# Kernel tuning notes

Measured on AMD Instinct MI355X. Metric: run time of the kernel, lower is better.

The kernel has to match this reference:

```python
import jax, jax.numpy as jnp
import numpy as np
import math

D = 300      # input_size
H = 5        # gat heads
NLAYERS = 2  # txt_gat_layer == img_gat_layer
N, L, K = 64, 1024, 64
E_TXT, E_IMG = 2048, 512


def _gat(x, edge_index, W, att_src, att_dst, bias):
    """PyG GATConv, concat=False (head mean), no self loops, eval mode (no dropout).
    x: (n, D); edge_index: (2, E); W: (D, H, D); att_*: (H, D); bias: (D,)."""
    n = x.shape[0]
    h = jnp.einsum('ld,dhe->lhe', x, W)                    # (n, H, D)
    src, dst = edge_index[0], edge_index[1]
    a_src = jnp.sum(h * att_src, axis=-1)                  # (n, H)
    a_dst = jnp.sum(h * att_dst, axis=-1)                  # (n, H)
    e = jax.nn.leaky_relu(a_src[src] + a_dst[dst], 0.2)    # (E, H)
    m = jax.ops.segment_max(e, dst, num_segments=n)        # per-target max
    m = jnp.where(jnp.isfinite(m), m, 0.0)                 # nodes w/o in-edges
    p = jnp.exp(e - m[dst])
    denom = jax.ops.segment_sum(p, dst, num_segments=n)
    alpha = p / (denom[dst] + 1e-16)                       # (E, H)
    out = jax.ops.segment_sum(alpha[:, :, None] * h[src], dst, num_segments=n)
    return out.mean(axis=1) + bias                         # (n, D)


def _layer_norm(x, g, b):
    mu = jnp.mean(x, axis=-1, keepdims=True)
    var = jnp.mean((x - mu) ** 2, axis=-1, keepdims=True)
    return (x - mu) / jnp.sqrt(var + 1e-5) * g + b


def _forward(t2, v2, score, edge_index, gnn_mask, key_padding_mask, np_mask,
             img_edge_index, txt_W, txt_att_src, txt_att_dst, txt_bias,
             img_W, img_att_src, img_att_dst, img_bias,
             w1, b1, w2, b2, ln_g, ln_b, lam=1.0):
    scale = 1.0 / jnp.sqrt(jnp.asarray(D, t2.dtype))
    q1 = jnp.einsum('nld,nkd->nlk', t2, v2) * scale        # (N, L, K)
    c = jnp.sum(score * t2, axis=1, keepdims=True)         # (N, 1, D)
    pa_token = t2 @ w1 + b1                                # (N, L)
    pa_token = jnp.where(key_padding_mask, -jnp.inf, pa_token)

    gat_txt = jax.vmap(_gat, in_axes=(0, 0, None, None, None, None))
    tnp = t2
    for i in range(NLAYERS):
        g = gat_txt(tnp, edge_index, txt_W[i], txt_att_src[i], txt_att_dst[i], txt_bias[i])
        g = jnp.where(gnn_mask[:, None, None], 0.0, g)     # masked graph -> zeros
        tnp = _layer_norm(jax.nn.relu(g), ln_g, ln_b)

    gat_img = jax.vmap(_gat, in_axes=(0, None, None, None, None, None))
    v3 = v2
    for i in range(NLAYERS):
        g = gat_img(v3, img_edge_index, img_W[i], img_att_src[i], img_att_dst[i], img_bias[i])
        v3 = _layer_norm(jax.nn.relu(g), ln_g, ln_b)

    tnp = jnp.concatenate([tnp, c], axis=1)                # (N, L+1, D)
    q2 = jnp.einsum('nld,nkd->nlk', tnp, v3) * scale       # (N, L+1, K)
    pa_np = tnp @ w2 + b2                                  # (N, L+1)
    pa_np = jnp.where(np_mask, -jnp.inf, pa_np)
    pa_np = jax.nn.softmax(pa_np * lam, axis=1)
    pa_tok = jax.nn.softmax(pa_token * lam, axis=1)
    a1 = jnp.sum(q1 * pa_tok[:, :, None], axis=1)          # (N, K)
    a2 = jnp.sum(q2 * pa_np[:, :, None], axis=1)           # (N, K)
    return jnp.concatenate([a1, a2], axis=1)               # (N, 2K)


def setup_inputs() -> dict:
    key = jax.random.key(0)
    ks = jax.random.split(key, 24)
    ws = 1.0 / math.sqrt(D)
    return {
        't2': jax.random.normal(ks[0], (N, L, D), jnp.float32),
        'v2': jax.random.normal(ks[1], (N, K, D), jnp.float32),
        'score': jax.random.uniform(ks[2], (N, L, D), jnp.float32),
        'edge_index': jax.random.randint(ks[3], (N, 2, E_TXT), 0, L),
        'gnn_mask': jnp.zeros((N,), bool),
        'key_padding_mask': jax.random.bernoulli(ks[4], 0.1, (N, L)),
        'np_mask': jax.random.bernoulli(ks[5], 0.1, (N, L + 1)),
        'img_edge_index': jax.random.randint(ks[6], (2, E_IMG), 0, K),
        'txt_W': jax.random.normal(ks[7], (NLAYERS, D, H, D), jnp.float32) * ws,
        'txt_att_src': jax.random.normal(ks[8], (NLAYERS, H, D), jnp.float32) * 0.1,
        'txt_att_dst': jax.random.normal(ks[9], (NLAYERS, H, D), jnp.float32) * 0.1,
        'txt_bias': jnp.zeros((NLAYERS, D), jnp.float32),
        'img_W': jax.random.normal(ks[10], (NLAYERS, D, H, D), jnp.float32) * ws,
        'img_att_src': jax.random.normal(ks[11], (NLAYERS, H, D), jnp.float32) * 0.1,
        'img_att_dst': jax.random.normal(ks[12], (NLAYERS, H, D), jnp.float32) * 0.1,
        'img_bias': jnp.zeros((NLAYERS, D), jnp.float32),
        'w1': jax.random.normal(ks[13], (D,), jnp.float32) * ws,
        'b1': jnp.zeros((), jnp.float32),
        'w2': jax.random.normal(ks[14], (D,), jnp.float32) * ws,
        'b2': jnp.zeros((), jnp.float32),
        'ln_g': jnp.ones((D,), jnp.float32),
        'ln_b': jnp.zeros((D,), jnp.float32),
    }


def reference(t2, v2, score, edge_index, gnn_mask, key_padding_mask, np_mask,
              img_edge_index, txt_W, txt_att_src, txt_att_dst, txt_bias,
              img_W, img_att_src, img_att_dst, img_bias,
              w1, b1, w2, b2, ln_g, ln_b):
    return _forward(t2, v2, score, edge_index, gnn_mask, key_padding_mask, np_mask,
                    img_edge_index, txt_W, txt_att_src, txt_att_dst, txt_bias,
                    img_W, img_att_src, img_att_dst, img_bias,
                    w1, b1, w2, b2, ln_g, ln_b)
```

## Files before the change

### kernel.cpp

```cpp
#include <hip/hip_runtime.h>
#include <hip/hip_bf16.h>
#include <math.h>

typedef __hip_bfloat16 bf16;
__device__ __forceinline__ float toF(float v){ return v; }
__device__ __forceinline__ float toF(bf16 v){ return __bfloat162float(v); }
__device__ __forceinline__ bf16 f2bf(float v){ return __float2bfloat16(v); }

#define D_    300
#define H_    5
#define NB    64
#define LL    1024
#define KK    64
#define ETXT  2048
#define EIMG  512
#define MAXDEG 128
#define KP    320
#define NP    1536

typedef __attribute__((ext_vector_type(8))) short short8;
typedef __attribute__((ext_vector_type(4))) float f32x4;

__device__ __forceinline__ int read_mask(const void* p, int i, int mode) {
  switch (mode) {
    case 1: return ((const unsigned short*)p)[i] != 0;
    case 2: return ((const unsigned char*)p)[i] != 0;
    case 3: { const unsigned int* w = (const unsigned int*)p;
              return (w[2*i] | w[2*i+1]) != 0; }
    default: return ((const unsigned int*)p)[i] != 0;
  }
}

__global__ void k_detect(const unsigned int* __restrict__ w, int nwords,
                         int* __restrict__ mode) {
  __shared__ unsigned int se[256], so[256];
  unsigned int oe = 0, oo = 0;
  for (int i = threadIdx.x; i < nwords; i += 256) {
    unsigned int v = w[i];
    if (i & 1) oo |= v; else oe |= v;
  }
  se[threadIdx.x] = oe; so[threadIdx.x] = oo;
  __syncthreads();
  for (int s = 128; s; s >>= 1) {
    if (threadIdx.x < s) { se[threadIdx.x] |= se[threadIdx.x+s]; so[threadIdx.x] |= so[threadIdx.x+s]; }
    __syncthreads();
  }
  if (threadIdx.x == 0) {
    unsigned int O = se[0] | so[0];
    int m = 0;
    if (O == 0u) m = 0;
    else if ((O & 0xFFFFu) == 0x3F80u) m = 1;
    else if ((O >> 16) == 0x3F80u && (O & 0xFFFFu) == 0u) m = 0;
    else if ((O >> 16) == 0x3FF0u) m = 3;
    else if (O <= 1u) m = (so[0] == 0u && se[0] != 0u) ? 3 : 0;
    else if ((O & 0xFEFEFEFEu) == 0u) m = 2;
    mode[0] = m;
  }
}

__global__ __launch_bounds__(256) void k_csr(const int* __restrict__ edges, int estride,
                                             int E, int nodes,
                                             int* __restrict__ rowptr, int rstride,
                                             int* __restrict__ col, int cstride) {
  int g = blockIdx.x, tid = threadIdx.x;
  __shared__ int cnt[1025];
  __shared__ int psum[257];
  const int* src = edges + (size_t)g * estride;
  const int* dst = src + E;
  for (int i = tid; i <= nodes; i += 256) cnt[i] = 0;
  __syncthreads();
  for (int e = tid; e < E; e += 256) atomicAdd(&cnt[dst[e]], 1);
  __syncthreads();
  int base = tid * 4;
  int loc = 0;
#pragma unroll
  for (int i = 0; i < 4; ++i) { int idx = base + i; if (idx < nodes) loc += cnt[idx]; }
  psum[tid + 1] = loc;
  if (tid == 0) psum[0] = 0;
  __syncthreads();
  if (tid == 0) { for (int i = 1; i <= 256; ++i) psum[i] += psum[i - 1]; }
  __syncthreads();
  int run = psum[tid];
  int starts[4];
#pragma unroll
  for (int i = 0; i < 4; ++i) {
    int idx = base + i;
    if (idx < nodes) { int c = cnt[idx]; starts[i] = run; run += c; }
  }
  __syncthreads();
#pragma unroll
  for (int i = 0; i < 4; ++i) {
    int idx = base + i;
    if (idx < nodes) { cnt[idx] = starts[i]; rowptr[(size_t)g * rstride + idx] = starts[i]; }
  }
  if (tid == 0) rowptr[(size_t)g * rstride + nodes] = E;
  __syncthreads();
  for (int e = tid; e < E; e += 256) {
    int pos = atomicAdd(&cnt[dst[e]], 1);
    col[(size_t)g * cstride + pos] = src[e];
  }
}

__global__ __launch_bounds__(1024) void k_c_part(const float* __restrict__ t2,
                                                 const float* __restrict__ score,
                                                 float* __restrict__ cpart) {
  int n = blockIdx.x, part = blockIdx.y;
  int lane = threadIdx.x & 63, ty = threadIdx.x >> 6;
  __shared__ float red[16][304];
  float acc[5] = {0.f, 0.f, 0.f, 0.f, 0.f};
  int l0 = part * 256;
  for (int l = l0 + ty; l < l0 + 256; l += 16) {
    const float* tp = t2 + ((size_t)n * LL + l) * D_;
    const float* sp = score + ((size_t)n * LL + l) * D_;
#pragma unroll
    for (int j = 0; j < 5; ++j) { int d = lane + 64 * j; if (d < D_) acc[j] += tp[d] * sp[d]; }
  }
#pragma unroll
  for (int j = 0; j < 5; ++j) { int d = lane + 64 * j; if (d < D_) red[ty][d] = acc[j]; }
  __syncthreads();
  for (int d = threadIdx.x; d < D_; d += 1024) {
    float s = 0.f;
#pragma unroll
    for (int t = 0; t < 16; ++t) s += red[t][d];
    cpart[((size_t)part * NB + n) * D_ + d] = s;
  }
}

__global__ void k_c_red(const float* __restrict__ cpart, float* __restrict__ c) {
  int idx = blockIdx.x * 256 + threadIdx.x;
  if (idx >= NB * D_) return;
  const int S = NB * D_;
  c[idx] = cpart[idx] + cpart[S + idx] + cpart[2 * S + idx] + cpart[3 * S + idx];
}

__device__ __forceinline__ float clamp_logit(float v) {
  if (!(v > -1e30f)) v = -1e30f;
  if (v > 1e30f) v = 1e30f;
  return v;
}

__global__ void k_logits_tok(const float* __restrict__ x, const float* __restrict__ w,
                             const float* __restrict__ b, const void* __restrict__ mask,
                             const int* __restrict__ mmode,
                             float* __restrict__ logits, int rows) {
  int row = blockIdx.x * blockDim.y + threadIdx.y;
  if (row >= rows) return;
  int lane = threadIdx.x;
  const float* xp = x + (size_t)row * D_;
  float acc = 0.f;
  for (int d = lane; d < D_; d += 64) acc += xp[d] * w[d];
#pragma unroll
  for (int off = 32; off; off >>= 1) acc += __shfl_down(acc, off);
  if (lane == 0) {
    float v = clamp_logit(acc + b[0]);
    if (read_mask(mask, row, mmode[0])) v = -INFINITY;
    logits[row] = v;
  }
}

__global__ void k_logits_np(const bf16* __restrict__ X, const float* __restrict__ c,
                            const float* __restrict__ w, const float* __restrict__ b,
                            const void* __restrict__ mask, const int* __restrict__ mmode,
                            float* __restrict__ logits) {
  int row = blockIdx.x * blockDim.y + threadIdx.y;
  if (row >= NB * (LL + 1)) return;
  int n = row / (LL + 1), l = row % (LL + 1);
  int lane = threadIdx.x;
  float acc = 0.f;
  if (l < LL) {
    const char* xp = (const char*)(X + ((size_t)n * LL + l) * D_);
#pragma unroll
    for (int t = 0; t < 3; ++t) {
      int d2 = lane + 64 * t;
      if (d2 < 150) {
        unsigned int u = *(const unsigned int*)(xp + d2 * 4);
        float2 wv = *(const float2*)&w[d2 * 2];
        acc += __uint_as_float(u << 16) * wv.x + __uint_as_float(u & 0xFFFF0000u) * wv.y;
      }
    }
  } else {
    const float* cp = c + n * D_;
    for (int d = lane; d < D_; d += 64) acc += cp[d] * w[d];
  }
#pragma unroll
  for (int off = 32; off; off >>= 1) acc += __shfl_down(acc, off);
  if (lane == 0) {
    float v = clamp_logit(acc + b[0]);
    if (read_mask(mask, row, mmode[0])) v = -INFINITY;
    logits[row] = v;
  }
}

__global__ __launch_bounds__(1024) void k_pa(const float* __restrict__ lg1,
                                             const float* __restrict__ lg2,
                                             float* __restrict__ pa1,
                                             float* __restrict__ pa2) {
  int b = blockIdx.x, tid = threadIdx.x;
  int which = b >> 6, n = b & 63;
  const float* lg = which ? (lg2 + (size_t)n * (LL + 1)) : (lg1 + (size_t)n * LL);
  float* pa = which ? (pa2 + (size_t)n * (LL + 1)) : (pa1 + (size_t)n * LL);
  __shared__ float red[16];
  __shared__ float stat;
  float v0 = lg[tid];
  float vx = (which && tid == 0) ? lg[LL] : -INFINITY;
  float m = fmaxf(v0, vx);
#pragma unroll
  for (int off = 32; off; off >>= 1) m = fmaxf(m, __shfl_xor(m, off));
  if ((tid & 63) == 0) red[tid >> 6] = m;
  __syncthreads();
  if (tid == 0) {
    float mm = red[0];
    for (int i = 1; i < 16; ++i) mm = fmaxf(mm, red[i]);
    stat = mm;
  }
  __syncthreads();
  float M = stat;
  if (!(M > -INFINITY && M < INFINITY)) M = 0.f;
  float p0 = __expf(v0 - M);
  float px = (which && tid == 0) ? __expf(vx - M) : 0.f;
  float s = p0 + px;
#pragma unroll
  for (int off = 32; off; off >>= 1) s += __shfl_xor(s, off);
  __syncthreads();
  if ((tid & 63) == 0) red[tid >> 6] = s;
  __syncthreads();
  if (tid == 0) {
    float ss = 0.f;
    for (int i = 0; i < 16; ++i) ss += red[i];
    stat = ss;
  }
  __syncthreads();
  float inv = (stat > 0.f) ? 1.f / stat : 0.f;
  pa[tid] = p0 * inv;
  if (which && tid == 0) pa[LL] = px * inv;
}

__global__ __launch_bounds__(1024) void k_u1part(const float* __restrict__ pa1,
                                                 const float* __restrict__ t2,
                                                 float* __restrict__ up) {
  int n = blockIdx.x, part = blockIdx.y;
  int lane = threadIdx.x & 63, ty = threadIdx.x >> 6;
  __shared__ float red[16][304];
  float acc[5] = {0.f, 0.f, 0.f, 0.f, 0.f};
  const float* pw = pa1 + (size_t)n * LL;
  int l0 = part * 256;
  for (int l = l0 + ty; l < l0 + 256; l += 16) {
    float w = pw[l];
    const float* tp = t2 + ((size_t)n * LL + l) * D_;
#pragma unroll
    for (int j = 0; j < 5; ++j) { int d = lane + 64 * j; if (d < D_) acc[j] += w * tp[d]; }
  }
#pragma unroll
  for (int j = 0; j < 5; ++j) { int d = lane + 64 * j; if (d < D_) red[ty][d] = acc[j]; }
  __syncthreads();
  for (int d = threadIdx.x; d < D_; d += 1024) {
    float s = 0.f;
#pragma unroll
    for (int t = 0; t < 16; ++t) s += red[t][d];
    up[((size_t)part * NB + n) * D_ + d] = s;
  }
}

__global__ __launch_bounds__(1024) void k_u2part(const float* __restrict__ pa2,
                                                 const bf16* __restrict__ X,
                                                 const float* __restrict__ c,
                                                 float* __restrict__ up) {
  int n = blockIdx.x, part = blockIdx.y;
  int lane = threadIdx.x & 63, ty = threadIdx.x >> 6;
  __shared__ float red[16][304];
  float acc[3][2] = {};
  const float* pw = pa2 + (size_t)n * (LL + 1);
  int l0 = part * 256;
  for (int l = l0 + ty; l < l0 + 256; l += 16) {
    float w = pw[l];
    const char* xp = (const char*)(X + ((size_t)n * LL + l) * D_);
#pragma unroll
    for (int t = 0; t < 3; ++t) {
      int d2 = lane + 64 * t;
      if (d2 < 150) {
        unsigned int u = *(const unsigned int*)(xp + d2 * 4);
        acc[t][0] += w * __uint_as_float(u << 16);
        acc[t][1] += w * __uint_as_float(u & 0xFFFF0000u);
      }
    }
  }
#pragma unroll
  for (int t = 0; t < 3; ++t) {
    int d2 = lane + 64 * t;
    if (d2 < 150) { red[ty][d2 * 2] = acc[t][0]; red[ty][d2 * 2 + 1] = acc[t][1]; }
  }
  __syncthreads();
  for (int d = threadIdx.x; d < D_; d += 1024) {
    float s = 0.f;
#pragma unroll
    for (int t = 0; t < 16; ++t) s += red[t][d];
    if (part == 3) s += pw[LL] * c[(size_t)n * D_ + d];
    up[((size_t)part * NB + n) * D_ + d] = s;
  }
}

__global__ void k_ured(const float* __restrict__ up1, const float* __restrict__ up2,
                       float* __restrict__ u1, float* __restrict__ u2) {
  int idx = blockIdx.x * 256 + threadIdx.x;
  if (idx >= NB * D_) return;
  const int S = NB * D_;
  u1[idx] = up1[idx] + up1[S + idx] + up1[2 * S + idx] + up1[3 * S + idx];
  u2[idx] = up2[idx] + up2[S + idx] + up2[2 * S + idx] + up2[3 * S + idx];
}

__global__ void k_wvec(const float* __restrict__ W, const float* __restrict__ att_src,
                       const float* __restrict__ att_dst, float* __restrict__ wsrc,
                       float* __restrict__ wdst) {
  int idx = blockIdx.x * blockDim.x + threadIdx.x;
  if (idx >= 2 * H_ * D_) return;
  int s = idx / (H_ * D_);
  int r = idx % (H_ * D_);
  int h = r / D_, d = r % D_;
  const float* att = (s ? att_dst : att_src) + h * D_;
  const float* Wp = W + (size_t)d * H_ * D_ + h * D_;
  float acc = 0.f;
  for (int e = 0; e < D_; ++e) acc += Wp[e] * att[e];
  (s ? wdst : wsrc)[h * D_ + d] = acc;
}

template <typename T>
__global__ void k_asrc(const T* __restrict__ x, const float* __restrict__ wsrc,
                       const float* __restrict__ wdst, float* __restrict__ a_src,
                       float* __restrict__ a_dst, int rows) {
  int row = blockIdx.x * blockDim.y + threadIdx.y;
  if (row >= rows) return;
  int lane = threadIdx.x;
  float xr[3][2];
#pragma unroll
  for (int t = 0; t < 3; ++t) {
    int d2 = lane + 64 * t;
    if (d2 < 150) {
      if constexpr (sizeof(T) == 4) {
        float2 v = *(const float2*)((const float*)x + (size_t)row * D_ + d2 * 2);
        xr[t][0] = v.x; xr[t][1] = v.y;
      } else {
        unsigned int u = *(const unsigned int*)((const char*)x + ((size_t)row * D_) * 2 + d2 * 4);
        xr[t][0] = __uint_as_float(u << 16); xr[t][1] = __uint_as_float(u & 0xFFFF0000u);
      }
    } else { xr[t][0] = 0.f; xr[t][1] = 0.f; }
  }
#pragma unroll
  for (int hh = 0; hh < H_; ++hh) {
    float as = 0.f, ad = 0.f;
#pragma unroll
    for (int t = 0; t < 3; ++t) {
      int d2 = lane + 64 * t;
      if (d2 < 150) {
        float2 ws = *(const float2*)&wsrc[hh * D_ + d2 * 2];
        float2 wd = *(const float2*)&wdst[hh * D_ + d2 * 2];
        as += xr[t][0] * ws.x + xr[t][1] * ws.y;
        ad += xr[t][0] * wd.x + xr[t][1] * wd.y;
      }
    }
#pragma unroll
    for (int off = 32; off; off >>= 1) { as += __shfl_down(as, off); ad += __shfl_down(ad, off); }
    if (lane == 0) { a_src[(size_t)row * H_ + hh] = as; a_dst[(size_t)row * H_ + hh] = ad; }
  }
}

template <typename T>
__global__ void k_packA(const T* __restrict__ src, bf16* __restrict__ Ap, int M) {
  int idx = blockIdx.x * 256 + threadIdx.x;
  if (idx >= M * KP) return;
  int m = idx / KP, k = idx - m * KP;
  Ap[idx] = (k < D_) ? f2bf(toF(src[(size_t)m * D_ + k])) : f2bf(0.f);
}

__global__ void k_packB(const float* __restrict__ B, bf16* __restrict__ Bp) {
  int idx = blockIdx.x * 256 + threadIdx.x;
  if (idx >= NP * KP) return;
  int j = idx / KP, k = idx - j * KP;
  float v = (k < D_ && j < H_ * D_) ? B[(size_t)k * (H_ * D_) + j] : 0.f;
  Bp[idx] = f2bf(v);
}

__global__ __launch_bounds__(256) void k_gemm_mfma(const bf16* __restrict__ Ap,
                                                   const bf16* __restrict__ Bp,
                                                   bf16* __restrict__ C, int M, int nrow) {
  __shared__ short As[128][40];
  __shared__ short Bs[128][40];
  int b = blockIdx.x;
  int xcd = b & 7, j = b >> 3;
  int rg = xcd + 8 * (j / 12);
  if (rg >= nrow) return;
  int m0 = rg * 128, n0 = (j % 12) * 128;
  int tid = threadIdx.x;
  int wave = tid >> 6, lane = tid & 63;
  int wr = (wave >> 1) * 64, wc = (wave & 1) * 64;
  f32x4 acc[4][4] = {};
  for (int k0 = 0; k0 < KP; k0 += 32) {
#pragma unroll
    for (int cc = 0; cc < 2; ++cc) {
      int c = tid + cc * 256;
      int m = c >> 2, ko = (c & 3) << 3;
      int row = m0 + m; if (row >= M) row = M - 1;
      *(uint4*)&As[m][ko] = *(const uint4*)(Ap + (size_t)row * KP + k0 + ko);
    }
#pragma unroll
    for (int cc = 0; cc < 2; ++cc) {
      int c = tid + cc * 256;
      int n = c >> 2, ko = (c & 3) << 3;
      *(uint4*)&Bs[n][ko] = *(const uint4*)(Bp + (size_t)(n0 + n) * KP + k0 + ko);
    }
    __syncthreads();
    int kq = (lane >> 4) << 3;
    short8 af[4], bfr[4];
#pragma unroll
    for (int i = 0; i < 4; ++i) af[i]  = *(const short8*)&As[wr + i * 16 + (lane & 15)][kq];
#pragma unroll
    for (int jj = 0; jj < 4; ++jj) bfr[jj] = *(const short8*)&Bs[wc + jj * 16 + (lane & 15)][kq];
#pragma unroll
    for (int i = 0; i < 4; ++i)
#pragma unroll
      for (int jj = 0; jj < 4; ++jj)
        acc[i][jj] = __builtin_amdgcn_mfma_f32_16x16x32_bf16(af[i], bfr[jj], acc[i][jj], 0, 0, 0);
    __syncthreads();
  }
  int cl = lane & 15, rq = (lane >> 4) << 2;
#pragma unroll
  for (int i = 0; i < 4; ++i) {
#pragma unroll
    for (int jj = 0; jj < 4; ++jj) {
      int col = n0 + wc + jj * 16 + cl;
#pragma unroll
      for (int r = 0; r < 4; ++r) {
        int row = m0 + wr + i * 16 + rq + r;
        if (row < M) C[(size_t)row * NP + col] = f2bf(acc[i][jj][r]);
      }
    }
  }
}

__global__ __launch_bounds__(256) void k_agg_ln(
    const bf16* __restrict__ h, const float* __restrict__ a_src, const float* __restrict__ a_dst,
    const int* __restrict__ rowptr, int rstride,
    const int* __restrict__ col, int cstride,
    int nodes, int lbpg, int swz, int gs,
    const void* __restrict__ gmask, const int* __restrict__ mmode, int g_off,
    const float* __restrict__ bias, const float* __restrict__ g_ln, const float* __restrict__ b_ln,
    bf16* __restrict__ xout) {
  int b = blockIdx.x;
  int wv = threadIdx.x >> 6, lane = threadIdx.x & 63;
  int g, nb;
  if (swz) { int j = b >> 3; g = (b & 7) + ((j >> lbpg) << 3); nb = j & ((1 << lbpg) - 1); }
  else     { g = b >> lbpg; nb = b & ((1 << lbpg) - 1); }
  int node = (nb << 2) + wv;
  if (g >= gs || node >= nodes) return;
  int gg = g_off + g;
  const int* rp = rowptr + (size_t)gg * rstride;
  int r0 = rp[node];
  int deg = rp[node + 1] - r0;
  if (deg > MAXDEG) deg = MAXDEG;
  const int* cp = col + (size_t)gg * cstride + r0;
  int row0 = g * nodes;
  const float* adr = a_dst + (size_t)(row0 + node) * H_;
  float ad[H_];
#pragma unroll
  for (int hh = 0; hh < H_; ++hh) ad[hh] = adr[hh];
  int d0 = deg < 64 ? deg : 64;
  int s0 = 0; float l0[H_];
  if (lane < d0) {
    s0 = cp[lane];
    const float* ap = a_src + (size_t)(row0 + s0) * H_;
#pragma unroll
    for (int hh = 0; hh < H_; ++hh) { float v = ap[hh] + ad[hh]; l0[hh] = v > 0.f ? v : 0.2f * v; }
  } else {
#pragma unroll
    for (int hh = 0; hh < H_; ++hh) l0[hh] = -INFINITY;
  }
  bool two = deg > 64;
  int s1 = 0; float l1[H_];
#pragma unroll
  for (int hh = 0; hh < H_; ++hh) l1[hh] = -INFINITY;
  if (two && lane < deg - 64) {
    s1 = cp[64 + lane];
    const float* ap = a_src + (size_t)(row0 + s1) * H_;
#pragma unroll
    for (int hh = 0; hh < H_; ++hh) { float v = ap[hh] + ad[hh]; l1[hh] = v > 0.f ? v : 0.2f * v; }
  }
  float al0[H_], al1[H_];
#pragma unroll
  for (int hh = 0; hh < H_; ++hh) {
    float m = two ? fmaxf(l0[hh], l1[hh]) : l0[hh];
    for (int off = 1; off < deg && off < 64; off <<= 1) m = fmaxf(m, __shfl_xor(m, off));
    m = __shfl(m, 0);
    float e0 = (lane < d0) ? __expf(l0[hh] - m) : 0.f;
    float e1 = (two && lane < deg - 64) ? __expf(l1[hh] - m) : 0.f;
    float s = e0 + e1;
    for (int off = 1; off < deg && off < 64; off <<= 1) s += __shfl_xor(s, off);
    s = __shfl(s, 0);
    float inv = 1.f / (s + 1e-16f);
    al0[hh] = e0 * inv;
    al1[hh] = e1 * inv;
  }
  float acc[3][2] = {};
  const char* hb = (const char*)h;
  for (int i = 0; i < deg; ++i) {
    int si; float aw[H_];
    if (i < 64) {
      si = __shfl(s0, i);
#pragma unroll
      for (int hh = 0; hh < H_; ++hh) aw[hh] = __shfl(al0[hh], i);
    } else {
      si = __shfl(s1, i - 64);
#pragma unroll
      for (int hh = 0; hh < H_; ++hh) aw[hh] = __shfl(al1[hh], i - 64);
    }
    const char* rb = hb + (size_t)(row0 + si) * (NP * 2);
#pragma unroll
    for (int t = 0; t < 3; ++t) {
      int d2 = lane + 64 * t;
      if (d2 < 150) {
#pragma unroll
        for (int hh = 0; hh < H_; ++hh) {
          unsigned int u = *(const unsigned int*)(rb + hh * (D_ * 2) + d2 * 4);
          float lo = __uint_as_float(u << 16);
          float hi = __uint_as_float(u & 0xFFFF0000u);
          acc[t][0] += aw[hh] * lo;
          acc[t][1] += aw[hh] * hi;
        }
      }
    }
  }
  int msk = gmask ? read_mask(gmask, gg, mmode[0]) : 0;
  float y[3][2];
  float ps = 0.f, pq = 0.f;
#pragma unroll
  for (int t = 0; t < 3; ++t) {
    int d2 = lane + 64 * t;
    float y0 = 0.f, y1 = 0.f;
    if (d2 < 150) {
      float2 bb = *(const float2*)&bias[d2 * 2];
      y0 = acc[t][0] * (1.f / H_) + bb.x;
      y1 = acc[t][1] * (1.f / H_) + bb.y;
      if (msk) { y0 = 0.f; y1 = 0.f; }
      y0 = fmaxf(y0, 0.f); y1 = fmaxf(y1, 0.f);
      ps += y0 + y1; pq += y0 * y0 + y1 * y1;
    }
    y[t][0] = y0; y[t][1] = y1;
  }
#pragma unroll
  for (int off = 1; off < 64; off <<= 1) { ps += __shfl_xor(ps, off); pq += __shfl_xor(pq, off); }
  float mu = ps * (1.f / 300.f);
  float var = pq * (1.f / 300.f) - mu * mu;
  var = fmaxf(var, 0.f);
  float rstd = rsqrtf(var + 1e-5f);
  char* orow = (char*)(xout + (size_t)(row0 + node) * D_);
#pragma unroll
  for (int t = 0; t < 3; ++t) {
    int d2 = lane + 64 * t;
    if (d2 < 150) {
      float2 gv = *(const float2*)&g_ln[d2 * 2];
      float2 bv = *(const float2*)&b_ln[d2 * 2];
      float o0 = (y[t][0] - mu) * rstd * gv.x + bv.x;
      float o1 = (y[t][1] - mu) * rstd * gv.y + bv.y;
      bf16 c0 = f2bf(o0), c1 = f2bf(o1);
      unsigned int u = ((unsigned int)*(unsigned short*)&c1 << 16) | (unsigned int)*(unsigned short*)&c0;
      *(unsigned int*)(orow + d2 * 4) = u;
    }
  }
}

__global__ void k_out(const float* __restrict__ u1, const float* __restrict__ u2,
                      const float* __restrict__ v2, const bf16* __restrict__ v3,
                      float* __restrict__ out) {
  int idx = blockIdx.x * blockDim.y + threadIdx.y;
  if (idx >= NB * KK) return;
  int n = idx / KK, k = idx - n * KK;
  int lane = threadIdx.x;
  const float* ap = v2 + (size_t)idx * D_;
  const bf16* bp = v3 + (size_t)idx * D_;
  const float* u1p = u1 + n * D_;
  const float* u2p = u2 + n * D_;
  float a1 = 0.f, a2 = 0.f;
  for (int d = lane; d < D_; d += 64) { a1 += u1p[d] * ap[d]; a2 += u2p[d] * toF(bp[d]); }
#pragma unroll
  for (int off = 32; off; off >>= 1) { a1 += __shfl_down(a1, off); a2 += __shfl_down(a2, off); }
  if (lane == 0) {
    const float scale = 0.05773502691896258f;
    out[(size_t)n * 2 * KK + k] = a1 * scale;
    out[(size_t)n * 2 * KK + KK + k] = a2 * scale;
  }
}

extern "C" void kernel_launch(void* const* d_in, const int* in_sizes, int n_in,
                              void* d_out, int out_size, void* d_ws, size_t ws_size,
                              hipStream_t stream) {
  const float* t2    = (const float*)d_in[0];
  const float* v2    = (const float*)d_in[1];
  const float* score = (const float*)d_in[2];
  const int*   eidx  = (const int*)d_in[3];
  const void*  gmask = d_in[4];
  const void*  kpm   = d_in[5];
  const void*  npm   = d_in[6];
  const int*   iedge = (const int*)d_in[7];
  const float* txtW  = (const float*)d_in[8];
  const float* txtAs = (const float*)d_in[9];
  const float* txtAd = (const float*)d_in[10];
  const float* txtB  = (const float*)d_in[11];
  const float* imgW  = (const float*)d_in[12];
  const float* imgAs = (const float*)d_in[13];
  const float* imgAd = (const float*)d_in[14];
  const float* imgB  = (const float*)d_in[15];
  const float* w1    = (const float*)d_in[16];
  const float* b1    = (const float*)d_in[17];
  const float* w2    = (const float*)d_in[18];
  const float* b2    = (const float*)d_in[19];
  const float* lng   = (const float*)d_in[20];
  const float* lnb   = (const float*)d_in[21];
  float* out = (float*)d_out;

  char* ws = (char*)d_ws;
  size_t off = 0;
  auto alloc = [&](size_t bytes) -> char* {
    char* p = ws + off;
    off += (bytes + 511) & ~(size_t)511;
    return p;
  };
  int*   mmode = (int*)alloc(64);
  float* c     = (float*)alloc((size_t)NB * D_ * 4);
  float* u1    = (float*)alloc((size_t)NB * D_ * 4);
  float* u2    = (float*)alloc((size_t)NB * D_ * 4);
  float* lg1   = (float*)alloc((size_t)NB * LL * 4);
  float* lg2   = (float*)alloc((size_t)NB * (LL + 1) * 4);
  float* pa1   = (float*)alloc((size_t)NB * LL * 4);
  float* pa2   = (float*)alloc((size_t)NB * (LL + 1) * 4);
  float* cpart = (float*)alloc((size_t)4 * NB * D_ * 4);
  float* up1   = (float*)alloc((size_t)4 * NB * D_ * 4);
  float* up2   = (float*)alloc((size_t)4 * NB * D_ * 4);
  float* wsrc  = (float*)alloc((size_t)H_ * D_ * 4);
  float* wdst  = (float*)alloc((size_t)H_ * D_ * 4);
  float* asrc  = (float*)alloc((size_t)NB * LL * H_ * 4);
  float* adst  = (float*)alloc((size_t)NB * LL * H_ * 4);
  int*   trp   = (int*)alloc((size_t)NB * (LL + 1) * 4);
  int*   tcol  = (int*)alloc((size_t)NB * ETXT * 4);
  int*   irp   = (int*)alloc((size_t)(KK + 1) * 4);
  int*   icol  = (int*)alloc((size_t)EIMG * 4);
  bf16*  X     = (bf16*)alloc((size_t)NB * LL * D_ * 2);
  bf16*  V     = (bf16*)alloc((size_t)NB * KK * D_ * 2);
  bf16*  Bp    = (bf16*)alloc((size_t)NP * KP * 2);
  size_t havail = (ws_size > off) ? (ws_size - off) : 0;
  char* hstart = ws + off;
  size_t per_g_txt = (size_t)LL * (KP + NP) * 2;
  int cg = (int)(havail / per_g_txt);
  if (cg < 1) cg = 1;
  if (cg > NB) cg = NB;
  size_t per_g_img = (size_t)KK * (KP + NP) * 2;
  int cgi = (int)(havail / per_g_img);
  if (cgi < 1) cgi = 1;
  if (cgi > NB) cgi = NB;

  dim3 b64x4(64, 4);

  k_detect<<<1, 256, 0, stream>>>((const unsigned int*)kpm, NB * LL / 4, mmode);

  k_csr<<<NB, 256, 0, stream>>>(eidx, 2 * ETXT, ETXT, LL, trp, LL + 1, tcol, ETXT);
  k_csr<<<1, 256, 0, stream>>>(iedge, 0, EIMG, KK, irp, 0, icol, 0);

  k_c_part<<<dim3(NB, 4), 1024, 0, stream>>>(t2, score, cpart);
  k_c_red<<<(NB * D_ + 255) / 256, 256, 0, stream>>>(cpart, c);
  k_logits_tok<<<(NB * LL + 3) / 4, b64x4, 0, stream>>>(t2, w1, b1, kpm, mmode, lg1, NB * LL);

  {
    bf16* Ap   = (bf16*)hstart;
    bf16* hbuf = (bf16*)(hstart + (size_t)cg * LL * KP * 2);
    for (int layer = 0; layer < 2; ++layer) {
      const float* W = txtW + (size_t)layer * D_ * H_ * D_;
      k_packB<<<(NP * KP + 255) / 256, 256, 0, stream>>>(W, Bp);
      k_wvec<<<(2 * H_ * D_ + 255) / 256, 256, 0, stream>>>(
          W, txtAs + layer * H_ * D_, txtAd + layer * H_ * D_, wsrc, wdst);
      for (int g0 = 0; g0 < NB; g0 += cg) {
        int gs = (cg < NB - g0) ? cg : (NB - g0);
        int M = gs * LL;
        bf16* Xout = X + (size_t)g0 * LL * D_;
        if (layer == 0) {
          const float* Xin = t2 + (size_t)g0 * LL * D_;
          k_packA<float><<<(M * KP + 255) / 256, 256, 0, stream>>>(Xin, Ap, M);
          k_asrc<float><<<(M + 3) / 4, b64x4, 0, stream>>>(Xin, wsrc, wdst, asrc, adst, M);
        } else {
          const bf16* Xin = X + (size_t)g0 * LL * D_;
          k_packA<bf16><<<(M * KP + 255) / 256, 256, 0, stream>>>(Xin, Ap, M);
          k_asrc<bf16><<<(M + 3) / 4, b64x4, 0, stream>>>(Xin, wsrc, wdst, asrc, adst, M);
        }
        int nrow = (M + 127) / 128;
        k_gemm_mfma<<<12 * 8 * ((nrow + 7) / 8), 256, 0, stream>>>(Ap, Bp, hbuf, M, nrow);
        int swz = (gs % 8 == 0);
        k_agg_ln<<<gs * (LL / 4), 256, 0, stream>>>(hbuf, asrc, adst, trp, LL + 1, tcol, ETXT,
                                                    LL, 8, swz, gs, gmask, mmode, g0,
                                                    txtB + layer * D_, lng, lnb, Xout);
      }
    }
  }

  {
    bf16* Ap   = (bf16*)hstart;
    bf16* hbuf = (bf16*)(hstart + (size_t)cgi * KK * KP * 2);
    for (int layer = 0; layer < 2; ++layer) {
      const float* W = imgW + (size_t)layer * D_ * H_ * D_;
      k_packB<<<(NP * KP + 255) / 256, 256, 0, stream>>>(W, Bp);
      k_wvec<<<(2 * H_ * D_ + 255) / 256, 256, 0, stream>>>(
          W, imgAs + layer * H_ * D_, imgAd + layer * H_ * D_, wsrc, wdst);
      for (int g0 = 0; g0 < NB; g0 += cgi) {
        int gs = (cgi < NB - g0) ? cgi : (NB - g0);
        int M = gs * KK;
        bf16* Vout = V + (size_t)g0 * KK * D_;
        if (layer == 0) {
          const float* Vin = v2 + (size_t)g0 * KK * D_;
          k_packA<float><<<(M * KP + 255) / 256, 256, 0, stream>>>(Vin, Ap, M);
          k_asrc<float><<<(M + 3) / 4, b64x4, 0, stream>>>(Vin, wsrc, wdst, asrc, adst, M);
        } else {
          const bf16* Vin = V + (size_t)g0 * KK * D_;
          k_packA<bf16><<<(M * KP + 255) / 256, 256, 0, stream>>>(Vin, Ap, M);
          k_asrc<bf16><<<(M + 3) / 4, b64x4, 0, stream>>>(Vin, wsrc, wdst, asrc, adst, M);
        }
        int nrow = (M + 127) / 128;
        k_gemm_mfma<<<12 * 8 * ((nrow + 7) / 8), 256, 0, stream>>>(Ap, Bp, hbuf, M, nrow);
        int swz = (gs % 8 == 0);
        k_agg_ln<<<gs * (KK / 4), 256, 0, stream>>>(hbuf, asrc, adst, irp, 0, icol, 0,
                                                    KK, 4, swz, gs, nullptr, mmode, 0,
                                                    imgB + layer * D_, lng, lnb, Vout);
      }
    }
  }

  k_logits_np<<<(NB * (LL + 1) + 3) / 4, b64x4, 0, stream>>>(X, c, w2, b2, npm, mmode, lg2);
  k_pa<<<128, 1024, 0, stream>>>(lg1, lg2, pa1, pa2);
  k_u1part<<<dim3(NB, 4), 1024, 0, stream>>>(pa1, t2, up1);
  k_u2part<<<dim3(NB, 4), 1024, 0, stream>>>(pa2, X, c, up2);
  k_ured<<<(NB * D_ + 255) / 256, 256, 0, stream>>>(up1, up2, u1, u2);
  k_out<<<(NB * KK + 3) / 4, b64x4, 0, stream>>>(u1, u2, v2, V, out);
}
```

Before: 1.079 ms.

## Use direct global-to-LDS loads in GEMM, vectorize packA and output stores

The MFMA GEMM now stages A and B tiles with global_load_lds 16-byte transfers straight into a flat unpadded LDS buffer, instead of loading through registers. The MFMA operands are swapped so each lane holds four consecutive output columns, which lets the epilogue write packed 8-byte bf16 stores rather than scalar ones. The A-pack kernel now converts and writes 8 elements per thread. The flat LDS layout drops the padding, which may cause bank conflicts on the fragment reads.

Result: slower. 1.108 ms (+2.7%).

```diff
diff --git a/kernel.cpp b/kernel.cpp
--- a/kernel.cpp
+++ b/kernel.cpp
@@ -20,6 +20,10 @@
 
 typedef __attribute__((ext_vector_type(8))) short short8;
 typedef __attribute__((ext_vector_type(4))) float f32x4;
+
+#define GLOAD16(g, l) __builtin_amdgcn_global_load_lds( \
+    (const __attribute__((address_space(1))) void*)(g), \
+    (__attribute__((address_space(3))) void*)(l), 16, 0, 0)
 
 __device__ __forceinline__ int read_mask(const void* p, int i, int mode) {
   switch (mode) {
@@ -364,11 +368,20 @@
 }
 
 template <typename T>
-__global__ void k_packA(const T* __restrict__ src, bf16* __restrict__ Ap, int M) {
+__global__ void k_packA8(const T* __restrict__ src, bf16* __restrict__ Ap, int M) {
   int idx = blockIdx.x * 256 + threadIdx.x;
-  if (idx >= M * KP) return;
-  int m = idx / KP, k = idx - m * KP;
-  Ap[idx] = (k < D_) ? f2bf(toF(src[(size_t)m * D_ + k])) : f2bf(0.f);
+  if (idx >= M * (KP / 8)) return;
+  int m = idx / (KP / 8), ci = idx - m * (KP / 8);
+  int k = ci * 8;
+  const T* sp = src + (size_t)m * D_ + k;
+  short8 o;
+#pragma unroll
+  for (int j = 0; j < 8; ++j) {
+    float v = (k + j < D_) ? toF(sp[j]) : 0.f;
+    bf16 b = f2bf(v);
+    o[j] = *(short*)&b;
+  }
+  *(short8*)&Ap[(size_t)idx * 8] = o;
 }
 
 __global__ void k_packB(const float* __restrict__ B, bf16* __restrict__ Bp) {
@@ -382,8 +395,7 @@
 __global__ __launch_bounds__(256) void k_gemm_mfma(const bf16* __restrict__ Ap,
                                                    const bf16* __restrict__ Bp,
                                                    bf16* __restrict__ C, int M, int nrow) {
-  __shared__ short As[128][40];
-  __shared__ short Bs[128][40];
+  __shared__ short St[8192];
   int b = blockIdx.x;
   int xcd = b & 7, j = b >> 3;
   int rg = xcd + 8 * (j / 12);
@@ -392,45 +404,49 @@
   int tid = threadIdx.x;
   int wave = tid >> 6, lane = tid & 63;
   int wr = (wave >> 1) * 64, wc = (wave & 1) * 64;
+  int cl = lane & 15, qw = lane >> 4;
+  int srow = tid >> 2;
+  int sch  = tid & 3;
   f32x4 acc[4][4] = {};
   for (int k0 = 0; k0 < KP; k0 += 32) {
 #pragma unroll
-    for (int cc = 0; cc < 2; ++cc) {
-      int c = tid + cc * 256;
-      int m = c >> 2, ko = (c & 3) << 3;
-      int row = m0 + m; if (row >= M) row = M - 1;
-      *(uint4*)&As[m][ko] = *(const uint4*)(Ap + (size_t)row * KP + k0 + ko);
-    }
-#pragma unroll
-    for (int cc = 0; cc < 2; ++cc) {
-      int c = tid + cc * 256;
-      int n = c >> 2, ko = (c & 3) << 3;
-      *(uint4*)&Bs[n][ko] = *(const uint4*)(Bp + (size_t)(n0 + n) * KP + k0 + ko);
+    for (int c = 0; c < 2; ++c) {
+      int ar = m0 + c * 64 + srow; if (ar >= M) ar = M - 1;
+      GLOAD16(Ap + (size_t)ar * KP + k0 + sch * 8, &St[c * 2048 + tid * 8]);
+    }
+#pragma unroll
+    for (int c = 0; c < 2; ++c) {
+      int br = n0 + c * 64 + srow;
+      GLOAD16(Bp + (size_t)br * KP + k0 + sch * 8, &St[4096 + c * 2048 + tid * 8]);
     }
     __syncthreads();
-    int kq = (lane >> 4) << 3;
+    int kq = qw << 3;
     short8 af[4], bfr[4];
 #pragma unroll
-    for (int i = 0; i < 4; ++i) af[i]  = *(const short8*)&As[wr + i * 16 + (lane & 15)][kq];
-#pragma unroll
-    for (int jj = 0; jj < 4; ++jj) bfr[jj] = *(const short8*)&Bs[wc + jj * 16 + (lane & 15)][kq];
+    for (int i = 0; i < 4; ++i) af[i]  = *(const short8*)&St[(wr + i * 16 + cl) * 32 + kq];
+#pragma unroll
+    for (int jj = 0; jj < 4; ++jj) bfr[jj] = *(const short8*)&St[4096 + (wc + jj * 16 + cl) * 32 + kq];
 #pragma unroll
     for (int i = 0; i < 4; ++i)
 #pragma unroll
       for (int jj = 0; jj < 4; ++jj)
-        acc[i][jj] = __builtin_amdgcn_mfma_f32_16x16x32_bf16(af[i], bfr[jj], acc[i][jj], 0, 0, 0);
+        acc[i][jj] = __builtin_amdgcn_mfma_f32_16x16x32_bf16(bfr[jj], af[i], acc[i][jj], 0, 0, 0);
     __syncthreads();
   }
-  int cl = lane & 15, rq = (lane >> 4) << 2;
 #pragma unroll
   for (int i = 0; i < 4; ++i) {
-#pragma unroll
-    for (int jj = 0; jj < 4; ++jj) {
-      int col = n0 + wc + jj * 16 + cl;
-#pragma unroll
-      for (int r = 0; r < 4; ++r) {
-        int row = m0 + wr + i * 16 + rq + r;
-        if (row < M) C[(size_t)row * NP + col] = f2bf(acc[i][jj][r]);
+    int row = m0 + wr + i * 16 + cl;
+    if (row < M) {
+      char* rowp = (char*)(C + (size_t)row * NP);
+#pragma unroll
+      for (int jj = 0; jj < 4; ++jj) {
+        int colb = n0 + wc + jj * 16 + qw * 4;
+        bf16 b0 = f2bf(acc[i][jj][0]), b1 = f2bf(acc[i][jj][1]);
+        bf16 b2 = f2bf(acc[i][jj][2]), b3 = f2bf(acc[i][jj][3]);
+        uint2 pv;
+        pv.x = ((unsigned int)*(unsigned short*)&b1 << 16) | (unsigned int)*(unsigned short*)&b0;
+        pv.y = ((unsigned int)*(unsigned short*)&b3 << 16) | (unsigned int)*(unsigned short*)&b2;
+        *(uint2*)(rowp + colb * 2) = pv;
       }
     }
   }
@@ -680,11 +696,11 @@
         bf16* Xout = X + (size_t)g0 * LL * D_;
         if (layer == 0) {
           const float* Xin = t2 + (size_t)g0 * LL * D_;
-          k_packA<float><<<(M * KP + 255) / 256, 256, 0, stream>>>(Xin, Ap, M);
+          k_packA8<float><<<(M * (KP / 8) + 255) / 256, 256, 0, stream>>>(Xin, Ap, M);
           k_asrc<float><<<(M + 3) / 4, b64x4, 0, stream>>>(Xin, wsrc, wdst, asrc, adst, M);
         } else {
           const bf16* Xin = X + (size_t)g0 * LL * D_;
-          k_packA<bf16><<<(M * KP + 255) / 256, 256, 0, stream>>>(Xin, Ap, M);
+          k_packA8<bf16><<<(M * (KP / 8) + 255) / 256, 256, 0, stream>>>(Xin, Ap, M);
           k_asrc<bf16><<<(M + 3) / 4, b64x4, 0, stream>>>(Xin, wsrc, wdst, asrc, adst, M);
         }
         int nrow = (M + 127) / 128;
@@ -711,11 +727,11 @@
         bf16* Vout = V + (size_t)g0 * KK * D_;
         if (layer == 0) {
           const float* Vin = v2 + (size_t)g0 * KK * D_;
-          k_packA<float><<<(M * KP + 255) / 256, 256, 0, stream>>>(Vin, Ap, M);
+          k_packA8<float><<<(M * (KP / 8) + 255) / 256, 256, 0, stream>>>(Vin, Ap, M);
           k_asrc<float><<<(M + 3) / 4, b64x4, 0, stream>>>(Vin, wsrc, wdst, asrc, adst, M);
         } else {
           const bf16* Vin = V + (size_t)g0 * KK * D_;
-          k_packA<bf16><<<(M * KP + 255) / 256, 256, 0, stream>>>(Vin, Ap, M);
+          k_packA8<bf16><<<(M * (KP / 8) + 255) / 256, 256, 0, stream>>>(Vin, Ap, M);
           k_asrc<bf16><<<(M + 3) / 4, b64x4, 0, stream>>>(Vin, wsrc, wdst, asrc, adst, M);
         }
         int nrow = (M + 127) / 128;
```
